# Kernel optimization log

Measured on AMD Instinct MI355X. Metric: run time of the kernel, lower is better.

## Reference

```python
import jax, jax.numpy as jnp
import numpy as np

B, N, D, H, E = 4, 2048, 512, 8, 512   # batch, seq, d_model, heads, dpb_embedding
D1 = 2 * D                              # expand_ratio * d_model (multiple of H)
HD = D1 // H                            # head dim for v/u space
GAMMA = 0.999


def _srms(x):
    # SimpleRMSNorm: x / (||x|| * d^-0.5 + eps)
    return x / (jnp.sqrt(jnp.mean(jnp.square(x), axis=-1, keepdims=True)) + 1e-8)


def setup_inputs() -> dict:
    key = jax.random.key(0)
    ks = jax.random.split(key, 10)
    s = 0.02

    def lin(k, i, o):
        kw, kb = jax.random.split(k)
        return (jax.random.normal(kw, (i, o), jnp.float32) * s,
                jax.random.normal(kb, (o,), jnp.float32) * s)

    Wu, bu = lin(ks[0], D, D1)
    Wv, bv = lin(ks[1], D, D1)
    Wo, bo = lin(ks[2], D1, D)
    Wp, bp = lin(ks[3], 1, E)        # DPB pos_proj: scalar position -> dpb_dim
    W1, b1 = lin(ks[4], E, E)
    W2, b2 = lin(ks[5], E, E)
    W3, b3 = lin(ks[6], E, E)
    Wz, bz = lin(ks[7], E, H * HD)   # DPB out: dpb_dim -> h*head_dim
    x = jax.random.normal(ks[8], (B, N, D), jnp.float32)
    return dict(x=x, Wu=Wu, bu=bu, Wv=Wv, bv=bv, Wo=Wo, bo=bo,
                Wp=Wp, bp=bp, W1=W1, b1=b1, W2=W2, b2=b2, W3=W3, b3=b3,
                Wz=Wz, bz=bz)


def reference(x, Wu, bu, Wv, bv, Wo, bo, Wp, bp, W1, b1, W2, b2, W3, b3, Wz, bz):
    shortcut = x                       # token_shift_type=-1, resi_param=False
    xn = _srms(x)                      # pre_norm = SimpleRMSNorm(d_model)
    u = jax.nn.silu(xn @ Wu + bu)      # b n d1
    v = jax.nn.silu(xn @ Wv + bv)      # b n d1
    b, n, _ = x.shape
    v = v.reshape(b, n, H, HD).transpose(0, 2, 1, 3)   # b h n d

    # --- DPB (Rpe MLP) on positions [0, 1, ..., n-1]; row 0 is the zero lag ---
    pos = jnp.arange(0, n, dtype=x.dtype).reshape(n, 1)  # par_type=1
    hcf = pos @ Wp + bp
    for W, bb in ((W1, b1), (W2, b2), (W3, b3)):         # non-residual layers
        hcf = jax.nn.relu(_srms(hcf)) @ W + bb
    coef = jax.nn.relu(_srms(hcf)) @ Wz + bz             # n, h*d
    coef = coef.reshape(n, H, HD).transpose(1, 0, 2)     # h n d
    zero = coef[:, :1]                                   # h 1 d  (lag 0)
    posc = coef[:, 1:]                                   # h n-1 d (lags 1..n-1)

    # fixed exponential decay gamma^i on positive lags (use_decay=True)
    decay = GAMMA ** jnp.arange(1, n, dtype=x.dtype)[None, :, None]
    # causal: negative lags are zero; rfft zero-pads to 2n
    a = jnp.concatenate([zero, decay * posc, zero], axis=1)  # h, n+1, d

    # --- causal Toeplitz matmul as circular conv of length 2n ---
    m = 2 * n
    fv = jnp.fft.rfft(v, m, axis=2)           # b h m/2+1 d
    fa = jnp.fft.rfft(a, m, axis=1)[None]     # 1 h m/2+1 d
    out = jnp.fft.irfft(fv * fa, m, axis=2)[:, :, :n]  # b h n d

    out = out.transpose(0, 2, 1, 3).reshape(b, n, H * HD)  # b n d1
    out = u * out                               # u-gating
    return out @ Wo + bo + shortcut             # output proj + residual
```

## Files before the change

### kernel.cpp

```cpp
#include <hip/hip_runtime.h>
#include <hip/hip_bf16.h>
#include <math.h>

using bf16 = __hip_bfloat16;
typedef short bf16x8 __attribute__((ext_vector_type(8)));
typedef float f32x4 __attribute__((ext_vector_type(4)));

#define GAMMA_LOG2 (-0.0014434688536725045f)

union Bf16Bits { bf16 h; unsigned short s; };
union VecU { uint4 q; unsigned short s[8]; };

__device__ inline unsigned short bf16_bits(float z)
{
    Bf16Bits u;
    u.h = __float2bfloat16(z);
    return u.s;
}

__device__ inline unsigned int packbf2(float a, float b)
{
    return (unsigned int)bf16_bits(a) | ((unsigned int)bf16_bits(b) << 16);
}

__device__ __forceinline__ void async_copy16(unsigned short* lds, const bf16* g)
{
    __builtin_amdgcn_global_load_lds(
        (const __attribute__((address_space(1))) unsigned int*)(const void*)g,
        (__attribute__((address_space(3))) unsigned int*)(void*)lds,
        16, 0, 0);
}

struct PrepArgs {
    const float* src[3];
    bf16* dst[3];
    int R[3];
    int C[3];
    int pfx[4];
};

__global__ void k_prologue(PrepArgs pa,
                           const float* __restrict__ W1, const float* __restrict__ W2,
                           const float* __restrict__ W3, const float* __restrict__ Wz,
                           bf16* __restrict__ Wf,
                           const float* __restrict__ x, bf16* __restrict__ xn)
{
    const int bidg = blockIdx.x;
    if (bidg < 1536) {
        __shared__ float tile[32][33];
        int bid = bidg;
        int seg = 0;
        while (bid >= pa.pfx[seg + 1]) ++seg;
        int local = bid - pa.pfx[seg];
        int R = pa.R[seg], C = pa.C[seg];
        int ctiles = C >> 5;
        int c0 = (local % ctiles) * 32, r0 = (local / ctiles) * 32;
        const float* in = pa.src[seg];
        bf16* out = pa.dst[seg];
        int tx = threadIdx.x & 31, ty = threadIdx.x >> 5;
#pragma unroll
        for (int i = 0; i < 4; ++i) {
            int r = r0 + ty + 8 * i;
            tile[ty + 8 * i][tx] = in[(size_t)r * C + c0 + tx];
        }
        __syncthreads();
#pragma unroll
        for (int i = 0; i < 4; ++i) {
            int cc = c0 + ty + 8 * i, rr = r0 + tx;
            out[(size_t)cc * R + rr] = __float2bfloat16(tile[tx][ty + 8 * i]);
        }
        return;
    }
    if (bidg < 2176) {
        int g = (bidg - 1536) * 256 + threadIdx.x;
        int unit = g >> 15;
        int idx = g & 32767;
        int lane = idx & 63;
        int nj = (idx >> 6) & 7;
        int ks = (idx >> 9) & 15;
        int wc = idx >> 13;
        int lm = lane & 15, lq = lane >> 4;
        int k0 = ks * 32 + lq * 8;
        const float* src;
        int N, o;
        if (unit < 3) {
            src = (unit == 0) ? W1 : (unit == 1) ? W2 : W3;
            N = 512;
            o = wc * 128 + nj * 16 + lm;
        } else {
            src = Wz;
            N = 1024;
            o = (unit - 3) * 512 + wc * 128 + nj * 16 + lm;
        }
        VecU v;
#pragma unroll
        for (int j = 0; j < 8; ++j)
            v.s[j] = bf16_bits(src[(size_t)(k0 + j) * N + o]);
        *(uint4*)(void*)(Wf + (size_t)g * 8) = v.q;
        return;
    }
    {
        int row = bidg - 2176, t = threadIdx.x;
        const float* xr = x + (size_t)row * 512;
        float a = xr[t], b = xr[t + 256];
        float v = a * a + b * b;
#pragma unroll
        for (int m = 32; m >= 1; m >>= 1) v += __shfl_xor(v, m, 64);
        __shared__ float ws[4];
        if ((t & 63) == 0) ws[t >> 6] = v;
        __syncthreads();
        float tot = ws[0] + ws[1] + ws[2] + ws[3];
        float s = 1.f / (sqrtf(tot * (1.f / 512.f)) + 1e-8f);
        bf16* o = xn + (size_t)row * 512;
        o[t] = __float2bfloat16(a * s);
        o[t + 256] = __float2bfloat16(b * s);
    }
}

__global__ void k_gate_transpose(const bf16* __restrict__ ud1t, const bf16* __restrict__ uv,
                                 bf16* __restrict__ out)
{
    __shared__ unsigned short tile[64][65];
    const int b = blockIdx.z;
    const int t = threadIdx.x;
    int c0 = blockIdx.x * 64, t0 = blockIdx.y * 64;
#pragma unroll
    for (int it = 0; it < 2; ++it) {
        int r = it * 32 + (t >> 3), cc = (t & 7) * 8;
        VecU v;
        v.q = *(const uint4*)(const void*)(ud1t + ((size_t)b * 1024 + c0 + r) * 2048 + t0 + cc);
#pragma unroll
        for (int i = 0; i < 8; ++i) tile[r][cc + i] = v.s[i];
    }
    __syncthreads();
#pragma unroll
    for (int it = 0; it < 2; ++it) {
        int tt = it * 32 + (t >> 3), cc = (t & 7) * 8;
        VecU vu;
        vu.q = *(const uint4*)(const void*)(uv + ((size_t)b * 2048 + t0 + tt) * 2048 + c0 + cc);
        VecU vo;
#pragma unroll
        for (int i = 0; i < 8; ++i) {
            Bf16Bits cv, uu;
            cv.s = tile[cc + i][tt];
            uu.s = vu.s[i];
            vo.s[i] = bf16_bits(__bfloat162float(cv.h) * __bfloat162float(uu.h));
        }
        *(uint4*)(void*)(out + ((size_t)b * 2048 + t0 + tt) * 1024 + c0 + cc) = vo.q;
    }
}

__global__ __launch_bounds__(1024, 1) void k_mlp(
    const float* __restrict__ Wp, const float* __restrict__ bp,
    const bf16* __restrict__ Wf,
    const float* __restrict__ b1, const float* __restrict__ b2,
    const float* __restrict__ b3, const float* __restrict__ bz,
    bf16* __restrict__ atb)
{
    __shared__ unsigned short X[32][520];
    __shared__ float sq2[32][33];
    __shared__ float red[16][32];
    __shared__ float scale[32];

    const int tid = threadIdx.x, lane = tid & 63, w = tid >> 6;
    const int lm = lane & 15, lq = lane >> 4;
    const int posBase = blockIdx.x * 32;

    {
        const int r = tid >> 5;
        const int cb = tid & 31;
        const int c0 = cb * 16;
        float vals[16];
        float ssq = 0.f;
        const float fp = (float)(posBase + r);
#pragma unroll
        for (int e = 0; e < 16; ++e) {
            float z = fp * Wp[c0 + e] + bp[c0 + e];
            vals[e] = z;
            ssq += z * z;
        }
        sq2[r][cb] = ssq;
        __syncthreads();
        float tot = 0.f;
#pragma unroll
        for (int i = 0; i < 32; ++i) tot += sq2[r][i];
        float s = 1.f / (sqrtf(tot * (1.f / 512.f)) + 1e-8f);
        unsigned int* xrow = (unsigned int*)&X[r][c0];
#pragma unroll
        for (int e = 0; e < 8; ++e)
            xrow[e] = packbf2(fmaxf(vals[2 * e] * s, 0.f), fmaxf(vals[2 * e + 1] * s, 0.f));
        __syncthreads();
    }

    const int wc = w >> 2, njb = (w & 3) * 2;

    auto layer_mm = [&](const bf16* Wu_, f32x4 (&acc)[2][2]) {
        const bf16* base = Wu_ + (size_t)wc * 65536 + (size_t)njb * 512 + (size_t)lane * 8;
        bf16x8 B0[2], B1[2], B2[2], B3[2];
#define LOADB(DST, KS)                                                        \
        DST[0] = *(const bf16x8*)(const void*)(base + (KS) * 4096);           \
        DST[1] = *(const bf16x8*)(const void*)(base + (KS) * 4096 + 512);
#define MMST(BUF, KS) {                                                       \
        bf16x8 af0 = *(const bf16x8*)(const void*)&X[lm][(KS) * 32 + lq * 8]; \
        bf16x8 af1 = *(const bf16x8*)(const void*)&X[16 + lm][(KS) * 32 + lq * 8]; \
        acc[0][0] = __builtin_amdgcn_mfma_f32_16x16x32_bf16(af0, BUF[0], acc[0][0], 0, 0, 0); \
        acc[0][1] = __builtin_amdgcn_mfma_f32_16x16x32_bf16(af0, BUF[1], acc[0][1], 0, 0, 0); \
        acc[1][0] = __builtin_amdgcn_mfma_f32_16x16x32_bf16(af1, BUF[0], acc[1][0], 0, 0, 0); \
        acc[1][1] = __builtin_amdgcn_mfma_f32_16x16x32_bf16(af1, BUF[1], acc[1][1], 0, 0, 0); }
        LOADB(B0, 0)  LOADB(B1, 1)  LOADB(B2, 2)
        LOADB(B3, 3)  MMST(B0, 0)
        LOADB(B0, 4)  MMST(B1, 1)
        LOADB(B1, 5)  MMST(B2, 2)
        LOADB(B2, 6)  MMST(B3, 3)
        LOADB(B3, 7)  MMST(B0, 4)
        LOADB(B0, 8)  MMST(B1, 5)
        LOADB(B1, 9)  MMST(B2, 6)
        LOADB(B2, 10) MMST(B3, 7)
        LOADB(B3, 11) MMST(B0, 8)
        LOADB(B0, 12) MMST(B1, 9)
        LOADB(B1, 13) MMST(B2, 10)
        LOADB(B2, 14) MMST(B3, 11)
        LOADB(B3, 15) MMST(B0, 12)
        MMST(B1, 13)
        MMST(B2, 14)
        MMST(B3, 15)
#undef LOADB
#undef MMST
    };

    const float* bs[3] = {b1, b2, b3};
    for (int l = 0; l < 3; ++l) {
        f32x4 acc[2][2];
#pragma unroll
        for (int mi = 0; mi < 2; ++mi)
#pragma unroll
            for (int i = 0; i < 2; ++i) acc[mi][i] = (f32x4){0.f, 0.f, 0.f, 0.f};
        layer_mm(Wf + (size_t)l * 262144, acc);
#pragma unroll
        for (int mi = 0; mi < 2; ++mi)
#pragma unroll
            for (int nj = 0; nj < 2; ++nj) {
                float bb = bs[l][w * 32 + nj * 16 + lm];
#pragma unroll
                for (int r = 0; r < 4; ++r) acc[mi][nj][r] += bb;
            }
        float pr[2][4] = {{0.f, 0.f, 0.f, 0.f}, {0.f, 0.f, 0.f, 0.f}};
#pragma unroll
        for (int mi = 0; mi < 2; ++mi)
#pragma unroll
            for (int nj = 0; nj < 2; ++nj)
#pragma unroll
                for (int r = 0; r < 4; ++r) pr[mi][r] += acc[mi][nj][r] * acc[mi][nj][r];
#pragma unroll
        for (int m = 1; m < 16; m <<= 1)
#pragma unroll
            for (int mi = 0; mi < 2; ++mi)
#pragma unroll
                for (int r = 0; r < 4; ++r) pr[mi][r] += __shfl_xor(pr[mi][r], m);
        if (lm == 0)
#pragma unroll
            for (int mi = 0; mi < 2; ++mi)
#pragma unroll
                for (int r = 0; r < 4; ++r) red[w][mi * 16 + lq * 4 + r] = pr[mi][r];
        __syncthreads();
        if (tid < 32) {
            float tot = 0.f;
#pragma unroll
            for (int wv = 0; wv < 16; ++wv) tot += red[wv][tid];
            scale[tid] = 1.f / (sqrtf(tot * (1.f / 512.f)) + 1e-8f);
        }
        __syncthreads();
#pragma unroll
        for (int mi = 0; mi < 2; ++mi)
#pragma unroll
            for (int nj = 0; nj < 2; ++nj) {
                int col = w * 32 + nj * 16 + lm;
#pragma unroll
                for (int r = 0; r < 4; ++r) {
                    int row = mi * 16 + lq * 4 + r;
                    float z = fmaxf(acc[mi][nj][r] * scale[row], 0.f);
                    *(unsigned short*)&X[row][col] = bf16_bits(z);
                }
            }
        __syncthreads();
    }

#pragma unroll
    for (int h = 0; h < 2; ++h) {
        f32x4 acc[2][2];
#pragma unroll
        for (int mi = 0; mi < 2; ++mi)
#pragma unroll
            for (int i = 0; i < 2; ++i) acc[mi][i] = (f32x4){0.f, 0.f, 0.f, 0.f};
        layer_mm(Wf + (size_t)(3 + h) * 262144, acc);
#pragma unroll
        for (int mi = 0; mi < 2; ++mi)
#pragma unroll
            for (int nj = 0; nj < 2; ++nj) {
                int col = h * 512 + w * 32 + nj * 16 + lm;
                float bb = bz[col];
                int pos0 = posBase + mi * 16 + lq * 4;
                float zs[4];
#pragma unroll
                for (int r = 0; r < 4; ++r)
                    zs[r] = (acc[mi][nj][r] + bb) * exp2f((float)(pos0 + r) * GAMMA_LOG2);
                uint2 o;
                o.x = packbf2(zs[0], zs[1]);
                o.y = packbf2(zs[2], zs[3]);
                *(uint2*)(void*)(atb + (size_t)col * 2048 + pos0) = o;
            }
    }
}

__global__ __launch_bounds__(256, 4) void k_uv(
    const bf16* __restrict__ A, const bf16* __restrict__ Bt,
    const float* __restrict__ bu, const float* __restrict__ bv,
    bf16* __restrict__ uvb, bf16* __restrict__ vtb)
{
    __shared__ unsigned short AB[2][2][128 * 32];

    const int tid = threadIdx.x, lane = tid & 63, w = tid >> 6;
    const int lm = lane & 15, lq = lane >> 4;
    const int gid = blockIdx.x;
    const int wm = (w >> 1) * 64, wn = (w & 1) * 64;
    const long rowBase = (long)(gid & 63) * 128, colBase = (long)(gid >> 6) * 128;

    const int srow = tid >> 2;
    const int sqz  = (tid & 3) ^ ((srow >> 1) & 3);
    const bf16* gA  = A  + (rowBase + srow) * 512 + sqz * 8;
    const bf16* gB  = Bt + (colBase + srow) * 512 + sqz * 8;
    const bf16* gA2 = gA + (size_t)64 * 512;
    const bf16* gB2 = gB + (size_t)64 * 512;
    const int ls0 = w * 512;
    const int ls1 = 2048 + w * 512;

    const int rdA = ((wm + lm) * 4 + (lq ^ ((lm >> 1) & 3))) * 8;
    const int rdB = ((wn + lm) * 4 + (lq ^ ((lm >> 1) & 3))) * 8;

    f32x4 acc[4][4];
    f32x4 zz = {0.f, 0.f, 0.f, 0.f};
#pragma unroll
    for (int i = 0; i < 4; ++i)
#pragma unroll
        for (int j = 0; j < 4; ++j) acc[i][j] = zz;

    async_copy16(&AB[0][0][ls0], gA);
    async_copy16(&AB[0][0][ls1], gA2);
    async_copy16(&AB[0][1][ls0], gB);
    async_copy16(&AB[0][1][ls1], gB2);
    __syncthreads();

#pragma unroll
    for (int t = 0; t < 16; ++t) {
        const int cur = t & 1;
        if (t < 15) {
            const int kk = (t + 1) * 32;
            async_copy16(&AB[cur ^ 1][0][ls0], gA + kk);
            async_copy16(&AB[cur ^ 1][0][ls1], gA2 + kk);
            async_copy16(&AB[cur ^ 1][1][ls0], gB + kk);
            async_copy16(&AB[cur ^ 1][1][ls1], gB2 + kk);
        }
        bf16x8 af[4], bfr[4];
#pragma unroll
        for (int mi = 0; mi < 4; ++mi)
            af[mi] = *(const bf16x8*)(const void*)&AB[cur][0][rdA + mi * 512];
#pragma unroll
        for (int nj = 0; nj < 4; ++nj)
            bfr[nj] = *(const bf16x8*)(const void*)&AB[cur][1][rdB + nj * 512];
#pragma unroll
        for (int mi = 0; mi < 4; ++mi)
#pragma unroll
            for (int nj = 0; nj < 4; ++nj)
                acc[mi][nj] = __builtin_amdgcn_mfma_f32_16x16x32_bf16(af[mi], bfr[nj], acc[mi][nj], 0, 0, 0);
        if (t < 15) __syncthreads();
    }

    const bool vhalf = colBase >= 1024;
    if (!vhalf) {
#pragma unroll
        for (int mi = 0; mi < 4; ++mi)
#pragma unroll
            for (int nj = 0; nj < 4; ++nj) {
                long col = colBase + wn + nj * 16 + lm;
                float bb = bu[col];
                long row0 = rowBase + wm + mi * 16 + lq * 4;
#pragma unroll
                for (int r = 0; r < 4; ++r) {
                    float z = acc[mi][nj][r] + bb;
                    z = z / (1.f + __expf(-z));
                    uvb[(size_t)(row0 + r) * 2048 + col] = __float2bfloat16(z);
                }
            }
    } else {
        __syncthreads();
        unsigned short* sh = &AB[0][0][0];
#pragma unroll
        for (int mi = 0; mi < 4; ++mi)
#pragma unroll
            for (int nj = 0; nj < 4; ++nj) {
                int c_local = wn + nj * 16 + lm;
                float bb = bv[colBase - 1024 + c_local];
                int t_local = wm + mi * 16 + lq * 4;
                float zs[4];
#pragma unroll
                for (int r = 0; r < 4; ++r) {
                    float z = acc[mi][nj][r] + bb;
                    zs[r] = z / (1.f + __expf(-z));
                }
                int p = (t_local + 8 * c_local) & 127;
                uint2 o;
                o.x = packbf2(zs[0], zs[1]);
                o.y = packbf2(zs[2], zs[3]);
                *(uint2*)(void*)&sh[c_local * 128 + p] = o;
            }
        __syncthreads();
        const int b   = (int)(rowBase >> 11);
        const int tb0 = (int)(rowBase & 2047);
        const long cb = colBase - 1024;
        const int cl = tid >> 4;
        const int ch = tid & 15;
#pragma unroll
        for (int it = 0; it < 8; ++it) {
            int c_local = it * 16 + cl;
            int p = (ch * 8 + 8 * c_local) & 127;
            uint4 q = *(const uint4*)(const void*)&sh[c_local * 128 + p];
            *(uint4*)(void*)(vtb + ((size_t)b * 1024 + cb + c_local) * 2048 + tb0 + ch * 8) = q;
        }
    }
}

__global__ __launch_bounds__(256, 4) void k_gemm_out2(
    const bf16* __restrict__ A, const bf16* __restrict__ Bt,
    const float* __restrict__ bias0, const float* __restrict__ addsrc,
    float* __restrict__ outp)
{
    __shared__ unsigned short As[2][64 * 32];
    __shared__ unsigned short Bs[2][128 * 32];

    const int tid = threadIdx.x, lane = tid & 63, w = tid >> 6;
    const int lm = lane & 15, lq = lane >> 4;
    const int wm = (w >> 1) * 32, wn = (w & 1) * 64;
    const long rowBase = (long)blockIdx.x * 64, colBase = (long)blockIdx.y * 128;

    const int srow = tid >> 2;
    const int sqz  = (tid & 3) ^ ((srow >> 1) & 3);
    const bf16* gA  = A  + (rowBase + srow) * 1024 + sqz * 8;
    const bf16* gB  = Bt + (colBase + srow) * 1024 + sqz * 8;
    const bf16* gB2 = gB + (size_t)64 * 1024;
    const int lsA = w * 512;
    const int lsB0 = w * 512, lsB1 = 2048 + w * 512;

    const int rdA = ((wm + lm) * 4 + (lq ^ ((lm >> 1) & 3))) * 8;
    const int rdB = ((wn + lm) * 4 + (lq ^ ((lm >> 1) & 3))) * 8;

    f32x4 acc[2][4];
    f32x4 zz = {0.f, 0.f, 0.f, 0.f};
#pragma unroll
    for (int i = 0; i < 2; ++i)
#pragma unroll
        for (int j = 0; j < 4; ++j) acc[i][j] = zz;

    async_copy16(&As[0][lsA], gA);
    async_copy16(&Bs[0][lsB0], gB);
    async_copy16(&Bs[0][lsB1], gB2);
    __syncthreads();

#pragma unroll
    for (int t = 0; t < 32; ++t) {
        const int cur = t & 1;
        if (t < 31) {
            const int kk = (t + 1) * 32;
            async_copy16(&As[cur ^ 1][lsA], gA + kk);
            async_copy16(&Bs[cur ^ 1][lsB0], gB + kk);
            async_copy16(&Bs[cur ^ 1][lsB1], gB2 + kk);
        }
        bf16x8 af[2], bfr[4];
#pragma unroll
        for (int mi = 0; mi < 2; ++mi)
            af[mi] = *(const bf16x8*)(const void*)&As[cur][rdA + mi * 512];
#pragma unroll
        for (int nj = 0; nj < 4; ++nj)
            bfr[nj] = *(const bf16x8*)(const void*)&Bs[cur][rdB + nj * 512];
#pragma unroll
        for (int mi = 0; mi < 2; ++mi)
#pragma unroll
            for (int nj = 0; nj < 4; ++nj)
                acc[mi][nj] = __builtin_amdgcn_mfma_f32_16x16x32_bf16(af[mi], bfr[nj], acc[mi][nj], 0, 0, 0);
        if (t < 31) __syncthreads();
    }

#pragma unroll
    for (int mi = 0; mi < 2; ++mi)
#pragma unroll
        for (int nj = 0; nj < 4; ++nj) {
            long col = colBase + wn + nj * 16 + lm;
            float bb = bias0[col];
#pragma unroll
            for (int r = 0; r < 4; ++r) {
                long row = rowBase + wm + mi * 16 + lq * 4 + r;
                size_t off = (size_t)row * 512 + col;
                outp[off] = acc[mi][nj][r] + bb + addsrc[off];
            }
        }
}

__global__ __launch_bounds__(256, 4) void k_conv_mfma(
    const bf16* __restrict__ vt, const bf16* __restrict__ at, bf16* __restrict__ ud1t)
{
    __shared__ unsigned short ash2[2][2068];
    __shared__ unsigned short vsh[4][3072];

    const int tid = threadIdx.x, lane = tid & 63, w = tid >> 6;
    const int c = blockIdx.x;

    {
        const unsigned short* asrc = (const unsigned short*)(at + (size_t)c * 2048);
        for (int i = tid; i < 2068; i += 256) {
#pragma unroll
            for (int k = 0; k < 2; ++k) {
                int src = 2047 - i - k;
                ash2[k][i] = (src >= 0) ? asrc[src] : (unsigned short)0;
            }
        }
    }
    {
        const bf16* vsrc = vt + ((size_t)w * 1024 + c) * 2048;
#pragma unroll
        for (int q = 0; q < 4; ++q) {
            int li = q * 64 + lane;
            int tile = li >> 1, hf = li & 1;
            *(uint4*)(void*)&vsh[w][tile * 24 + hf * 8] =
                *(const uint4*)(const void*)(vsrc + li * 8);
        }
    }
    __syncthreads();

    const int lm = lane & 15, lq = lane >> 4;
    const int h = lq >> 1, p0 = (lq & 1) * 8;
    const int kcopy = (lm + 1) & 1;
    const int base = 31 - 16 * h - lm + p0 - kcopy;
    const unsigned int* aw = (const unsigned int*)(void*)&ash2[kcopy][0] + (base >> 1);
    const unsigned short* vw = &vsh[w][0];

    f32x4 acc[8];
    f32x4 zz = {0.f, 0.f, 0.f, 0.f};
#pragma unroll
    for (int i = 0; i < 8; ++i) acc[i] = zz;
    const bf16x8 zfrag = (bf16x8)(short)0;

    for (int d2 = 0; d2 < 16; d2 += 2) {
        bf16x8 vf[8];
        const int tb = lm - d2 - h;
        {
            int T = tb > 0 ? tb : 0;
            bf16x8 f = *(const bf16x8*)(const void*)(vw + T * 24 + p0);
            vf[0] = (tb < 0) ? zfrag : f;
        }
#pragma unroll
        for (int dl = 1; dl < 8; ++dl)
            vf[dl] = *(const bf16x8*)(const void*)(vw + (dl * 16 + tb) * 24 + p0);

#pragma unroll
        for (int dt = 0; dt < 8; ++dt) {
            const int m16 = (63 - ((dt * 16 + d2) >> 1)) * 16;
            union { unsigned int u[4]; bf16x8 v; } af;
            af.u[0] = aw[m16 + 0];
            af.u[1] = aw[m16 + 1];
            af.u[2] = aw[m16 + 2];
            af.u[3] = aw[m16 + 3];
#pragma unroll
            for (int dl = 0; dl < 8 - dt; ++dl)
                acc[dt + dl] = __builtin_amdgcn_mfma_f32_16x16x32_bf16(af.v, vf[dl], acc[dt + dl], 0, 0, 0);
        }
    }

    __syncthreads();
    float* stg = (float*)(void*)((char*)(void*)&ash2[0][0] + w * 1024);
    bf16* dst = ud1t + ((size_t)w * 1024 + c) * 2048;
#pragma unroll
    for (int jg = 0; jg < 8; ++jg) {
        *(f32x4*)(void*)&stg[lm * 16 + lq * 4] = acc[jg];
        f32x4 vv = *(const f32x4*)(const void*)&stg[lane * 4];
        uint2 o;
        o.x = packbf2(vv.x, vv.y);
        o.y = packbf2(vv.z, vv.w);
        *(uint2*)(void*)(dst + jg * 256 + lane * 4) = o;
    }
}

extern "C" void kernel_launch(void* const* d_in, const int* in_sizes, int n_in,
                              void* d_out, int out_size, void* d_ws, size_t ws_size,
                              hipStream_t stream)
{
    const float* x  = (const float*)d_in[0];
    const float* Wu = (const float*)d_in[1];
    const float* bu = (const float*)d_in[2];
    const float* Wv = (const float*)d_in[3];
    const float* bv = (const float*)d_in[4];
    const float* Wo = (const float*)d_in[5];
    const float* bo = (const float*)d_in[6];
    const float* Wp = (const float*)d_in[7];
    const float* bp = (const float*)d_in[8];
    const float* W1 = (const float*)d_in[9];
    const float* b1 = (const float*)d_in[10];
    const float* W2 = (const float*)d_in[11];
    const float* b2 = (const float*)d_in[12];
    const float* W3 = (const float*)d_in[13];
    const float* b3 = (const float*)d_in[14];
    const float* Wz = (const float*)d_in[15];
    const float* bz = (const float*)d_in[16];

    char* p = (char*)d_ws;
    auto carve = [&](size_t bytes) { void* q = (void*)p; p += (bytes + 255) & ~(size_t)255; return q; };
    bf16*  xn   = (bf16*)carve((size_t)8192 * 512 * 2);
    bf16*  Wuvt = (bf16*)carve((size_t)2048 * 512 * 2);
    bf16*  Wot  = (bf16*)carve((size_t)512 * 1024 * 2);
    bf16*  Wf   = (bf16*)carve((size_t)5 * 262144 * 2);
    bf16*  uvb  = (bf16*)carve((size_t)8192 * 2048 * 2);
    bf16*  ud1  = (bf16*)carve((size_t)8192 * 1024 * 2);
    bf16*  vtb  = (bf16*)carve((size_t)4 * 1024 * 2048 * 2);
    bf16*  atb  = (bf16*)carve((size_t)1024 * 2048 * 2);
    bf16*  ud1t = (bf16*)carve((size_t)4 * 1024 * 2048 * 2);

    PrepArgs pa;
    const float* srcs[3] = {Wu, Wv, Wo};
    bf16* dsts[3] = {Wuvt, Wuvt + (size_t)1024 * 512, Wot};
    int Rs[3] = {512, 512, 1024};
    int Cs[3] = {1024, 1024, 512};
    int acc_t = 0;
    for (int i = 0; i < 3; ++i) {
        pa.src[i] = srcs[i]; pa.dst[i] = dsts[i]; pa.R[i] = Rs[i]; pa.C[i] = Cs[i];
        pa.pfx[i] = acc_t;
        acc_t += (Rs[i] / 32) * (Cs[i] / 32);
    }
    pa.pfx[3] = acc_t;
    k_prologue<<<1536 + 640 + 8192, 256, 0, stream>>>(pa, W1, W2, W3, Wz, Wf, x, xn);

    k_mlp<<<64, 1024, 0, stream>>>(Wp, bp, Wf, b1, b2, b3, bz, atb);

    k_uv<<<1024, 256, 0, stream>>>(xn, Wuvt, bu, bv, uvb, vtb);

    k_conv_mfma<<<dim3(1024), 256, 0, stream>>>(vtb, atb, ud1t);

    k_gate_transpose<<<dim3(16, 32, 4), 256, 0, stream>>>(ud1t, uvb, ud1);

    k_gemm_out2<<<dim3(128, 4), 256, 0, stream>>>(ud1, Wot, bo, x, (float*)d_out);
}
```

Baseline: 231.2 us.

## Fuse DPB MLP and UV projection GEMM into one 1024-thread launch

Merges the positional MLP kernel (64 blocks) and the u/v projection GEMM into a single launch in which the first 64 blocks run the MLP and the rest run the GEMM, with shared memory unioned between the two roles. The GEMM is rewritten for 1024-thread blocks, with 16 waves each computing a 32x32 sub-tile of the 128x128 tile. Each thread now issues a single async copy per k-step for either A or B. The aim is to overlap the small, latency-bound MLP with the GEMM and remove one launch boundary. The risk is that smaller per-wave tiles give less register reuse, and 1024-thread blocks may lower scheduling flexibility and occupancy.

```diff
diff --git a/kernel.cpp b/kernel.cpp
--- a/kernel.cpp
+++ b/kernel.cpp
@@ -150,227 +150,230 @@
     }
 }
 
-__global__ __launch_bounds__(1024, 1) void k_mlp(
+struct SharedFused {
+    union {
+        struct { unsigned short AB[2][2][4096]; } g;
+        struct {
+            unsigned short X[32][520];
+            float sq2[32][33];
+            float red[16][32];
+            float scale[32];
+        } m;
+    };
+};
+
+__global__ __launch_bounds__(1024, 2) void k_uv_mlp2(
+    const bf16* __restrict__ A, const bf16* __restrict__ Bt,
+    const float* __restrict__ bu, const float* __restrict__ bv,
     const float* __restrict__ Wp, const float* __restrict__ bp,
     const bf16* __restrict__ Wf,
     const float* __restrict__ b1, const float* __restrict__ b2,
     const float* __restrict__ b3, const float* __restrict__ bz,
-    bf16* __restrict__ atb)
-{
-    __shared__ unsigned short X[32][520];
-    __shared__ float sq2[32][33];
-    __shared__ float red[16][32];
-    __shared__ float scale[32];
+    bf16* __restrict__ uvb, bf16* __restrict__ vtb, bf16* __restrict__ atb)
+{
+    __shared__ SharedFused sh;
 
     const int tid = threadIdx.x, lane = tid & 63, w = tid >> 6;
     const int lm = lane & 15, lq = lane >> 4;
-    const int posBase = blockIdx.x * 32;
-
-    {
-        const int r = tid >> 5;
-        const int cb = tid & 31;
-        const int c0 = cb * 16;
-        float vals[16];
-        float ssq = 0.f;
-        const float fp = (float)(posBase + r);
-#pragma unroll
-        for (int e = 0; e < 16; ++e) {
-            float z = fp * Wp[c0 + e] + bp[c0 + e];
-            vals[e] = z;
-            ssq += z * z;
-        }
-        sq2[r][cb] = ssq;
-        __syncthreads();
-        float tot = 0.f;
-#pragma unroll
-        for (int i = 0; i < 32; ++i) tot += sq2[r][i];
-        float s = 1.f / (sqrtf(tot * (1.f / 512.f)) + 1e-8f);
-        unsigned int* xrow = (unsigned int*)&X[r][c0];
-#pragma unroll
-        for (int e = 0; e < 8; ++e)
-            xrow[e] = packbf2(fmaxf(vals[2 * e] * s, 0.f), fmaxf(vals[2 * e + 1] * s, 0.f));
-        __syncthreads();
-    }
-
-    const int wc = w >> 2, njb = (w & 3) * 2;
-
-    auto layer_mm = [&](const bf16* Wu_, f32x4 (&acc)[2][2]) {
-        const bf16* base = Wu_ + (size_t)wc * 65536 + (size_t)njb * 512 + (size_t)lane * 8;
-        bf16x8 B0[2], B1[2], B2[2], B3[2];
+
+    if (blockIdx.x < 64) {
+        unsigned short (&X)[32][520] = sh.m.X;
+        float (&sq2)[32][33] = sh.m.sq2;
+        float (&red)[16][32] = sh.m.red;
+        float (&scale)[32] = sh.m.scale;
+        const int posBase = blockIdx.x * 32;
+
+        {
+            const int r = tid >> 5;
+            const int cb = tid & 31;
+            const int c0 = cb * 16;
+            float vals[16];
+            float ssq = 0.f;
+            const float fp = (float)(posBase + r);
+#pragma unroll
+            for (int e = 0; e < 16; ++e) {
+                float z = fp * Wp[c0 + e] + bp[c0 + e];
+                vals[e] = z;
+                ssq += z * z;
+            }
+            sq2[r][cb] = ssq;
+            __syncthreads();
+            float tot = 0.f;
+#pragma unroll
+            for (int i = 0; i < 32; ++i) tot += sq2[r][i];
+            float s = 1.f / (sqrtf(tot * (1.f / 512.f)) + 1e-8f);
+            unsigned int* xrow = (unsigned int*)&X[r][c0];
+#pragma unroll
+            for (int e = 0; e < 8; ++e)
+                xrow[e] = packbf2(fmaxf(vals[2 * e] * s, 0.f), fmaxf(vals[2 * e + 1] * s, 0.f));
+            __syncthreads();
+        }
+
+        const int wc = w >> 2, njb = (w & 3) * 2;
+
+        auto layer_mm = [&](const bf16* Wu_, f32x4 (&acc)[2][2]) {
+            const bf16* base = Wu_ + (size_t)wc * 65536 + (size_t)njb * 512 + (size_t)lane * 8;
+            bf16x8 B0[2], B1[2], B2[2], B3[2];
 #define LOADB(DST, KS)                                                        \
-        DST[0] = *(const bf16x8*)(const void*)(base + (KS) * 4096);           \
-        DST[1] = *(const bf16x8*)(const void*)(base + (KS) * 4096 + 512);
+            DST[0] = *(const bf16x8*)(const void*)(base + (KS) * 4096);       \
+            DST[1] = *(const bf16x8*)(const void*)(base + (KS) * 4096 + 512);
 #define MMST(BUF, KS) {                                                       \
-        bf16x8 af0 = *(const bf16x8*)(const void*)&X[lm][(KS) * 32 + lq * 8]; \
-        bf16x8 af1 = *(const bf16x8*)(const void*)&X[16 + lm][(KS) * 32 + lq * 8]; \
-        acc[0][0] = __builtin_amdgcn_mfma_f32_16x16x32_bf16(af0, BUF[0], acc[0][0], 0, 0, 0); \
-        acc[0][1] = __builtin_amdgcn_mfma_f32_16x16x32_bf16(af0, BUF[1], acc[0][1], 0, 0, 0); \
-        acc[1][0] = __builtin_amdgcn_mfma_f32_16x16x32_bf16(af1, BUF[0], acc[1][0], 0, 0, 0); \
-        acc[1][1] = __builtin_amdgcn_mfma_f32_16x16x32_bf16(af1, BUF[1], acc[1][1], 0, 0, 0); }
-        LOADB(B0, 0)  LOADB(B1, 1)  LOADB(B2, 2)
-        LOADB(B3, 3)  MMST(B0, 0)
-        LOADB(B0, 4)  MMST(B1, 1)
-        LOADB(B1, 5)  MMST(B2, 2)
-        LOADB(B2, 6)  MMST(B3, 3)
-        LOADB(B3, 7)  MMST(B0, 4)
-        LOADB(B0, 8)  MMST(B1, 5)
-        LOADB(B1, 9)  MMST(B2, 6)
-        LOADB(B2, 10) MMST(B3, 7)
-        LOADB(B3, 11) MMST(B0, 8)
-        LOADB(B0, 12) MMST(B1, 9)
-        LOADB(B1, 13) MMST(B2, 10)
-        LOADB(B2, 14) MMST(B3, 11)
-        LOADB(B3, 15) MMST(B0, 12)
-        MMST(B1, 13)
-        MMST(B2, 14)
-        MMST(B3, 15)
+            bf16x8 af0 = *(const bf16x8*)(const void*)&X[lm][(KS) * 32 + lq * 8]; \
+            bf16x8 af1 = *(const bf16x8*)(const void*)&X[16 + lm][(KS) * 32 + lq * 8]; \
+            acc[0][0] = __builtin_amdgcn_mfma_f32_16x16x32_bf16(af0, BUF[0], acc[0][0], 0, 0, 0); \
+            acc[0][1] = __builtin_amdgcn_mfma_f32_16x16x32_bf16(af0, BUF[1], acc[0][1], 0, 0, 0); \
+            acc[1][0] = __builtin_amdgcn_mfma_f32_16x16x32_bf16(af1, BUF[0], acc[1][0], 0, 0, 0); \
+            acc[1][1] = __builtin_amdgcn_mfma_f32_16x16x32_bf16(af1, BUF[1], acc[1][1], 0, 0, 0); }
+            LOADB(B0, 0)  LOADB(B1, 1)  LOADB(B2, 2)
+            LOADB(B3, 3)  MMST(B0, 0)
+            LOADB(B0, 4)  MMST(B1, 1)
+            LOADB(B1, 5)  MMST(B2, 2)
+            LOADB(B2, 6)  MMST(B3, 3)
+            LOADB(B3, 7)  MMST(B0, 4)
+            LOADB(B0, 8)  MMST(B1, 5)
+            LOADB(B1, 9)  MMST(B2, 6)
+            LOADB(B2, 10) MMST(B3, 7)
+            LOADB(B3, 11) MMST(B0, 8)
+            LOADB(B0, 12) MMST(B1, 9)
+            LOADB(B1, 13) MMST(B2, 10)
+            LOADB(B2, 14) MMST(B3, 11)
+            LOADB(B3, 15) MMST(B0, 12)
+            MMST(B1, 13)
+            MMST(B2, 14)
+            MMST(B3, 15)
 #undef LOADB
 #undef MMST
-    };
-
-    const float* bs[3] = {b1, b2, b3};
-    for (int l = 0; l < 3; ++l) {
-        f32x4 acc[2][2];
-#pragma unroll
-        for (int mi = 0; mi < 2; ++mi)
-#pragma unroll
-            for (int i = 0; i < 2; ++i) acc[mi][i] = (f32x4){0.f, 0.f, 0.f, 0.f};
-        layer_mm(Wf + (size_t)l * 262144, acc);
-#pragma unroll
-        for (int mi = 0; mi < 2; ++mi)
-#pragma unroll
-            for (int nj = 0; nj < 2; ++nj) {
-                float bb = bs[l][w * 32 + nj * 16 + lm];
-#pragma unroll
-                for (int r = 0; r < 4; ++r) acc[mi][nj][r] += bb;
+        };
+
+        const float* bs[3] = {b1, b2, b3};
+        for (int l = 0; l < 3; ++l) {
+            f32x4 acc[2][2];
+#pragma unroll
+            for (int mi = 0; mi < 2; ++mi)
+#pragma unroll
+                for (int i = 0; i < 2; ++i) acc[mi][i] = (f32x4){0.f, 0.f, 0.f, 0.f};
+            layer_mm(Wf + (size_t)l * 262144, acc);
+#pragma unroll
+            for (int mi = 0; mi < 2; ++mi)
+#pragma unroll
+                for (int nj = 0; nj < 2; ++nj) {
+                    float bb = bs[l][w * 32 + nj * 16 + lm];
+#pragma unroll
+                    for (int r = 0; r < 4; ++r) acc[mi][nj][r] += bb;
+                }
+            float pr[2][4] = {{0.f, 0.f, 0.f, 0.f}, {0.f, 0.f, 0.f, 0.f}};
+#pragma unroll
+            for (int mi = 0; mi < 2; ++mi)
+#pragma unroll
+                for (int nj = 0; nj < 2; ++nj)
+#pragma unroll
+                    for (int r = 0; r < 4; ++r) pr[mi][r] += acc[mi][nj][r] * acc[mi][nj][r];
+#pragma unroll
+            for (int m = 1; m < 16; m <<= 1)
+#pragma unroll
+                for (int mi = 0; mi < 2; ++mi)
+#pragma unroll
+                    for (int r = 0; r < 4; ++r) pr[mi][r] += __shfl_xor(pr[mi][r], m);
+            if (lm == 0)
+#pragma unroll
+                for (int mi = 0; mi < 2; ++mi)
+#pragma unroll
+                    for (int r = 0; r < 4; ++r) red[w][mi * 16 + lq * 4 + r] = pr[mi][r];
+            __syncthreads();
+            if (tid < 32) {
+                float tot = 0.f;
+#pragma unroll
+                for (int wv = 0; wv < 16; ++wv) tot += red[wv][tid];
+                scale[tid] = 1.f / (sqrtf(tot * (1.f / 512.f)) + 1e-8f);
             }
-        float pr[2][4] = {{0.f, 0.f, 0.f, 0.f}, {0.f, 0.f, 0.f, 0.f}};
-#pragma unroll
-        for (int mi = 0; mi < 2; ++mi)
-#pragma unroll
-            for (int nj = 0; nj < 2; ++nj)
-#pragma unroll
-                for (int r = 0; r < 4; ++r) pr[mi][r] += acc[mi][nj][r] * acc[mi][nj][r];
-#pragma unroll
-        for (int m = 1; m < 16; m <<= 1)
+            __syncthreads();
 #pragma unroll
             for (int mi = 0; mi < 2; ++mi)
 #pragma unroll
-                for (int r = 0; r < 4; ++r) pr[mi][r] += __shfl_xor(pr[mi][r], m);
-        if (lm == 0)
+                for (int nj = 0; nj < 2; ++nj) {
+                    int col = w * 32 + nj * 16 + lm;
+#pragma unroll
+                    for (int r = 0; r < 4; ++r) {
+                        int row = mi * 16 + lq * 4 + r;
+                        float z = fmaxf(acc[mi][nj][r] * scale[row], 0.f);
+                        *(unsigned short*)&X[row][col] = bf16_bits(z);
+                    }
+                }
+            __syncthreads();
+        }
+
+#pragma unroll
+        for (int h = 0; h < 2; ++h) {
+            f32x4 acc[2][2];
 #pragma unroll
             for (int mi = 0; mi < 2; ++mi)
 #pragma unroll
-                for (int r = 0; r < 4; ++r) red[w][mi * 16 + lq * 4 + r] = pr[mi][r];
-        __syncthreads();
-        if (tid < 32) {
-            float tot = 0.f;
-#pragma unroll
-            for (int wv = 0; wv < 16; ++wv) tot += red[wv][tid];
-            scale[tid] = 1.f / (sqrtf(tot * (1.f / 512.f)) + 1e-8f);
-        }
-        __syncthreads();
-#pragma unroll
-        for (int mi = 0; mi < 2; ++mi)
-#pragma unroll
-            for (int nj = 0; nj < 2; ++nj) {
-                int col = w * 32 + nj * 16 + lm;
-#pragma unroll
-                for (int r = 0; r < 4; ++r) {
-                    int row = mi * 16 + lq * 4 + r;
-                    float z = fmaxf(acc[mi][nj][r] * scale[row], 0.f);
-                    *(unsigned short*)&X[row][col] = bf16_bits(z);
+                for (int i = 0; i < 2; ++i) acc[mi][i] = (f32x4){0.f, 0.f, 0.f, 0.f};
+            layer_mm(Wf + (size_t)(3 + h) * 262144, acc);
+#pragma unroll
+            for (int mi = 0; mi < 2; ++mi)
+#pragma unroll
+                for (int nj = 0; nj < 2; ++nj) {
+                    int col = h * 512 + w * 32 + nj * 16 + lm;
+                    float bb = bz[col];
+                    int pos0 = posBase + mi * 16 + lq * 4;
+                    float zs[4];
+#pragma unroll
+                    for (int r = 0; r < 4; ++r)
+                        zs[r] = (acc[mi][nj][r] + bb) * exp2f((float)(pos0 + r) * GAMMA_LOG2);
+                    uint2 o;
+                    o.x = packbf2(zs[0], zs[1]);
+                    o.y = packbf2(zs[2], zs[3]);
+                    *(uint2*)(void*)(atb + (size_t)col * 2048 + pos0) = o;
                 }
-            }
-        __syncthreads();
-    }
-
-#pragma unroll
-    for (int h = 0; h < 2; ++h) {
-        f32x4 acc[2][2];
-#pragma unroll
-        for (int mi = 0; mi < 2; ++mi)
-#pragma unroll
-            for (int i = 0; i < 2; ++i) acc[mi][i] = (f32x4){0.f, 0.f, 0.f, 0.f};
-        layer_mm(Wf + (size_t)(3 + h) * 262144, acc);
-#pragma unroll
-        for (int mi = 0; mi < 2; ++mi)
-#pragma unroll
-            for (int nj = 0; nj < 2; ++nj) {
-                int col = h * 512 + w * 32 + nj * 16 + lm;
-                float bb = bz[col];
-                int pos0 = posBase + mi * 16 + lq * 4;
-                float zs[4];
-#pragma unroll
-                for (int r = 0; r < 4; ++r)
-                    zs[r] = (acc[mi][nj][r] + bb) * exp2f((float)(pos0 + r) * GAMMA_LOG2);
-                uint2 o;
-                o.x = packbf2(zs[0], zs[1]);
-                o.y = packbf2(zs[2], zs[3]);
-                *(uint2*)(void*)(atb + (size_t)col * 2048 + pos0) = o;
-            }
-    }
-}
-
-__global__ __launch_bounds__(256, 4) void k_uv(
-    const bf16* __restrict__ A, const bf16* __restrict__ Bt,
-    const float* __restrict__ bu, const float* __restrict__ bv,
-    bf16* __restrict__ uvb, bf16* __restrict__ vtb)
-{
-    __shared__ unsigned short AB[2][2][128 * 32];
-
-    const int tid = threadIdx.x, lane = tid & 63, w = tid >> 6;
-    const int lm = lane & 15, lq = lane >> 4;
-    const int gid = blockIdx.x;
-    const int wm = (w >> 1) * 64, wn = (w & 1) * 64;
+        }
+        return;
+    }
+
+    unsigned short (&AB)[2][2][4096] = sh.g.AB;
+
+    const int gid = (int)blockIdx.x - 64;
+    const int wm = (w >> 2) * 32, wn = (w & 3) * 32;
     const long rowBase = (long)(gid & 63) * 128, colBase = (long)(gid >> 6) * 128;
 
-    const int srow = tid >> 2;
-    const int sqz  = (tid & 3) ^ ((srow >> 1) & 3);
-    const bf16* gA  = A  + (rowBase + srow) * 512 + sqz * 8;
-    const bf16* gB  = Bt + (colBase + srow) * 512 + sqz * 8;
-    const bf16* gA2 = gA + (size_t)64 * 512;
-    const bf16* gB2 = gB + (size_t)64 * 512;
-    const int ls0 = w * 512;
-    const int ls1 = 2048 + w * 512;
+    const int isB = tid >> 9;
+    const int ci  = tid & 511;
+    const int srow = ci >> 2;
+    const int sqz  = (ci & 3) ^ ((srow >> 1) & 3);
+    const bf16* gsrc = (isB ? (Bt + (colBase + srow) * 512)
+                            : (A  + (rowBase + srow) * 512)) + sqz * 8;
+    unsigned short* ld0 = &AB[0][isB][(w & 7) * 512];
+    unsigned short* ld1 = &AB[1][isB][(w & 7) * 512];
 
     const int rdA = ((wm + lm) * 4 + (lq ^ ((lm >> 1) & 3))) * 8;
     const int rdB = ((wn + lm) * 4 + (lq ^ ((lm >> 1) & 3))) * 8;
 
-    f32x4 acc[4][4];
+    f32x4 acc[2][2];
     f32x4 zz = {0.f, 0.f, 0.f, 0.f};
 #pragma unroll
-    for (int i = 0; i < 4; ++i)
-#pragma unroll
-        for (int j = 0; j < 4; ++j) acc[i][j] = zz;
-
-    async_copy16(&AB[0][0][ls0], gA);
-    async_copy16(&AB[0][0][ls1], gA2);
-    async_copy16(&AB[0][1][ls0], gB);
-    async_copy16(&AB[0][1][ls1], gB2);
+    for (int i = 0; i < 2; ++i)
+#pragma unroll
+        for (int j = 0; j < 2; ++j) acc[i][j] = zz;
+
+    async_copy16(ld0, gsrc);
     __syncthreads();
 
 #pragma unroll
     for (int t = 0; t < 16; ++t) {
         const int cur = t & 1;
-        if (t < 15) {
-            const int kk = (t + 1) * 32;
-            async_copy16(&AB[cur ^ 1][0][ls0], gA + kk);
-            async_copy16(&AB[cur ^ 1][0][ls1], gA2 + kk);
-            async_copy16(&AB[cur ^ 1][1][ls0], gB + kk);
-            async_copy16(&AB[cur ^ 1][1][ls1], gB2 + kk);
-        }
-        bf16x8 af[4], bfr[4];
-#pragma unroll
-        for (int mi = 0; mi < 4; ++mi)
+        if (t < 15)
+            async_copy16(cur ? ld0 : ld1, gsrc + (t + 1) * 32);
+        bf16x8 af[2], bfr[2];
+#pragma unroll
+        for (int mi = 0; mi < 2; ++mi)
             af[mi] = *(const bf16x8*)(const void*)&AB[cur][0][rdA + mi * 512];
 #pragma unroll
-        for (int nj = 0; nj < 4; ++nj)
+        for (int nj = 0; nj < 2; ++nj)
             bfr[nj] = *(const bf16x8*)(const void*)&AB[cur][1][rdB + nj * 512];
 #pragma unroll
-        for (int mi = 0; mi < 4; ++mi)
-#pragma unroll
-            for (int nj = 0; nj < 4; ++nj)
+        for (int mi = 0; mi < 2; ++mi)
+#pragma unroll
+            for (int nj = 0; nj < 2; ++nj)
                 acc[mi][nj] = __builtin_amdgcn_mfma_f32_16x16x32_bf16(af[mi], bfr[nj], acc[mi][nj], 0, 0, 0);
         if (t < 15) __syncthreads();
     }
@@ -378,9 +381,9 @@
     const bool vhalf = colBase >= 1024;
     if (!vhalf) {
 #pragma unroll
-        for (int mi = 0; mi < 4; ++mi)
-#pragma unroll
-            for (int nj = 0; nj < 4; ++nj) {
+        for (int mi = 0; mi < 2; ++mi)
+#pragma unroll
+            for (int nj = 0; nj < 2; ++nj) {
                 long col = colBase + wn + nj * 16 + lm;
                 float bb = bu[col];
                 long row0 = rowBase + wm + mi * 16 + lq * 4;
@@ -393,11 +396,11 @@
             }
     } else {
         __syncthreads();
-        unsigned short* sh = &AB[0][0][0];
-#pragma unroll
-        for (int mi = 0; mi < 4; ++mi)
-#pragma unroll
-            for (int nj = 0; nj < 4; ++nj) {
+        unsigned short* shv = &AB[0][0][0];
+#pragma unroll
+        for (int mi = 0; mi < 2; ++mi)
+#pragma unroll
+            for (int nj = 0; nj < 2; ++nj) {
                 int c_local = wn + nj * 16 + lm;
                 float bb = bv[colBase - 1024 + c_local];
                 int t_local = wm + mi * 16 + lq * 4;
@@ -411,7 +414,7 @@
                 uint2 o;
                 o.x = packbf2(zs[0], zs[1]);
                 o.y = packbf2(zs[2], zs[3]);
-                *(uint2*)(void*)&sh[c_local * 128 + p] = o;
+                *(uint2*)(void*)&shv[c_local * 128 + p] = o;
             }
         __syncthreads();
         const int b   = (int)(rowBase >> 11);
@@ -420,10 +423,10 @@
         const int cl = tid >> 4;
         const int ch = tid & 15;
 #pragma unroll
-        for (int it = 0; it < 8; ++it) {
-            int c_local = it * 16 + cl;
+        for (int it = 0; it < 2; ++it) {
+            int c_local = it * 64 + cl;
             int p = (ch * 8 + 8 * c_local) & 127;
-            uint4 q = *(const uint4*)(const void*)&sh[c_local * 128 + p];
+            uint4 q = *(const uint4*)(const void*)&shv[c_local * 128 + p];
             *(uint4*)(void*)(vtb + ((size_t)b * 1024 + cb + c_local) * 2048 + tb0 + ch * 8) = q;
         }
     }
@@ -636,9 +639,8 @@
     pa.pfx[3] = acc_t;
     k_prologue<<<1536 + 640 + 8192, 256, 0, stream>>>(pa, W1, W2, W3, Wz, Wf, x, xn);
 
-    k_mlp<<<64, 1024, 0, stream>>>(Wp, bp, Wf, b1, b2, b3, bz, atb);
-
-    k_uv<<<1024, 256, 0, stream>>>(xn, Wuvt, bu, bv, uvb, vtb);
+    k_uv_mlp2<<<1088, 1024, 0, stream>>>(xn, Wuvt, bu, bv, Wp, bp,
+                                         Wf, b1, b2, b3, bz, uvb, vtb, atb);
 
     k_conv_mfma<<<dim3(1024), 256, 0, stream>>>(vtb, atb, ud1t);
 
```

Measured after the change: 210.9 us. -8.8%, faster.
